# Performance work log

Measured on AMD Instinct MI355X. Metric: run time of the kernel, lower is better.

## Reference

```python
import jax, jax.numpy as jnp
import numpy as np

BN_EPS = 1e-5


def _knn_idx(pos, k):
    # pos: (B, 3, N). Nearest-k by squared euclidean distance (self included).
    sq = jnp.sum(pos * pos, axis=1)                        # (B, N)
    inner = jnp.einsum('bcn,bcm->bnm', pos, pos)           # (B, N, N)
    neg_dist = 2.0 * inner - sq[:, :, None] - sq[:, None, :]
    _, idx = jax.lax.top_k(neg_dist, k)                    # (B, N, k)
    return idx


def setup_inputs() -> dict:
    key = jax.random.key(0)
    k1, k2, k3 = jax.random.split(key, 3)
    B, C, N, K, D = 4, 64, 8192, 16, 64
    return {
        'x': jax.random.normal(k1, (B, C, N), dtype=jnp.float32),
        'pos': jax.random.normal(k2, (B, 3, N), dtype=jnp.float32),
        'spectral_filter': jax.random.normal(k3, (K, C, D), dtype=jnp.float32),
        'gamma': jnp.ones((D,), dtype=jnp.float32),
        'beta': jnp.zeros((D,), dtype=jnp.float32),
    }


def reference(x, pos, spectral_filter, gamma, beta):
    k = spectral_filter.shape[0]
    idx = _knn_idx(pos, k)                                  # (B, N, k) int32
    # gather neighbors: nb[b, c, n, j] = x[b, c, idx[b, n, j]]
    nb = jax.vmap(lambda xf, ii: xf[:, ii])(x, idx)         # (B, C, N, k)
    edge = nb - x[:, :, :, None]                            # (B, C, N, k)
    # per-k small GEMM: 'bnkc,kcd->bnd' (channel dim is axis 1 here)
    out = jnp.einsum('bcnk,kcd->bnd', edge, spectral_filter)
    out = out.transpose(0, 2, 1)                            # (B, D, N)
    # BatchNorm1d, training mode (biased variance over batch and points)
    mean = jnp.mean(out, axis=(0, 2), keepdims=True)
    var = jnp.var(out, axis=(0, 2), keepdims=True)
    out = (out - mean) * jax.lax.rsqrt(var + BN_EPS)
    return out * gamma[None, :, None] + beta[None, :, None]
```

## Files before the change

kernel.cpp:

```cpp
#include <hip/hip_runtime.h>
#include <hip/hip_bf16.h>

#define NPTS 8192
#define NQ   32768
#define KNN  16
#define SCAP 112

#define OFF_XT   0
#define OFF_FBIG (8*1024*1024)
#define OFF_SUMS (OFF_FBIG + 278528)
#define OFF_IDX  (OFF_SUMS + 512)
#define OFF_PRE  (OFF_IDX + 2*1024*1024)
#define OFF_SQ   OFF_PRE

__device__ __forceinline__ float sq3(float x, float y, float z) {
    #pragma clang fp contract(off)
    float xx = x * x;
    float yy = y * y;
    float zz = z * z;
    return (xx + yy) + zz;
}
__device__ __forceinline__ float negd2(float qx, float qy, float qz, float sqn,
                                       float mx, float my, float mz, float sqm) {
    #pragma clang fp contract(off)
    float p0 = qx * mx;
    float inn = __builtin_fmaf(qz, mz, __builtin_fmaf(qy, my, p0));
    float t = 2.0f * inn;
    float u = t - sqn;
    return u - sqm;
}
#define KEY_EPS2 2.0e-3f

__global__ __launch_bounds__(256) void k_prep(const float* __restrict__ x,
                                              const float* __restrict__ F,
                                              const float* __restrict__ pos,
                                              float* __restrict__ xT,
                                              float* __restrict__ Fb,
                                              float* __restrict__ sums,
                                              float* __restrict__ sqa) {
    int bid = blockIdx.x;
    if (bid < 512) {
        __shared__ float tile[64][65];
        int lane = threadIdx.x & 63, wid = threadIdx.x >> 6;
        int b = bid >> 7, nt = bid & 127;
        int n0 = nt * 64;
        for (int rr = 0; rr < 16; ++rr) {
            int c = wid * 16 + rr;
            tile[c][lane] = x[((size_t)b * 64 + c) * NPTS + n0 + lane];
        }
        __syncthreads();
        for (int rr = 0; rr < 16; ++rr) {
            int r = wid * 16 + rr;
            xT[((size_t)(b * NPTS + n0 + r)) * 64 + lane] = tile[lane][r];
        }
    } else if (bid < 528) {
        int j = bid - 512;
        for (int e = threadIdx.x; e < 4096; e += 256)
            Fb[j * 4096 + e] = F[j * 4096 + e];
    } else if (bid == 528) {
        for (int e = threadIdx.x; e < 4096; e += 256) {
            float s = 0.f;
            for (int k = 0; k < 16; ++k) s += F[k * 4096 + e];
            Fb[16 * 4096 + e] = -s;
        }
    } else if (bid == 529) {
        if (threadIdx.x < 128) sums[threadIdx.x] = 0.f;
    } else {
        int g = (bid - 530) * 256 + threadIdx.x;
        int b = g >> 13, n = g & (NPTS - 1);
        const float* pb = pos + (size_t)b * 3 * NPTS;
        sqa[g] = sq3(pb[n], pb[NPTS + n], pb[2 * NPTS + n]);
    }
}

__global__ __launch_bounds__(256, 4) void k_knn(const float* __restrict__ pos,
                                                const float* __restrict__ sqa,
                                                int* __restrict__ idxo) {
    __shared__ int            cnt[32];
    __shared__ unsigned short sidx[32][SCAP];
    __shared__ float          skey[32][SCAP];
    __shared__ int            outI[32][16];
    int t = threadIdx.x, lane = t & 63, wid = t >> 6;
    int qblk = blockIdx.x * 32;
    int b = qblk >> 13;
    const float* px = pos + (size_t)b * 3 * NPTS;
    const float* py = px + NPTS;
    const float* pz = py + NPTS;
    const float* sb = sqa + (size_t)b * NPTS;
    int n0 = (qblk & (NPTS - 1)) + wid * 8;

    float qxs[8], qys[8], qzs[8], sqs[8], tqx[8], tqy[8], tqz[8];
    #pragma unroll
    for (int i = 0; i < 8; ++i) {
        qxs[i] = px[n0 + i]; qys[i] = py[n0 + i]; qzs[i] = pz[n0 + i];
        sqs[i] = sb[n0 + i];
        tqx[i] = 2.0f * qxs[i]; tqy[i] = 2.0f * qys[i]; tqz[i] = 2.0f * qzs[i];
    }
    if (lane < 8) cnt[wid * 8 + lane] = 0;
    if (lane < 16) {
        #pragma unroll
        for (int i = 0; i < 8; ++i) outI[wid * 8 + i][lane] = n0 + i;
    }

    float lm[8];
    #pragma unroll
    for (int i = 0; i < 8; ++i) lm[i] = -3.4e38f;
    for (int it = 0; it < 32; ++it) {
        int m = it * 256 + lane * 4;
        float4 X = *(const float4*)(px + m);
        float4 Y = *(const float4*)(py + m);
        float4 Z = *(const float4*)(pz + m);
        float4 S = *(const float4*)(sb + m);
        #pragma unroll
        for (int i = 0; i < 8; ++i) {
            float a0 = __builtin_fmaf(tqx[i], X.x, __builtin_fmaf(tqy[i], Y.x, __builtin_fmaf(tqz[i], Z.x, -S.x)));
            float a1 = __builtin_fmaf(tqx[i], X.y, __builtin_fmaf(tqy[i], Y.y, __builtin_fmaf(tqz[i], Z.y, -S.y)));
            float a2 = __builtin_fmaf(tqx[i], X.z, __builtin_fmaf(tqy[i], Y.z, __builtin_fmaf(tqz[i], Z.z, -S.z)));
            float a3 = __builtin_fmaf(tqx[i], X.w, __builtin_fmaf(tqy[i], Y.w, __builtin_fmaf(tqz[i], Z.w, -S.w)));
            float m012 = fmaxf(fmaxf(a0, a1), a2);
            lm[i] = fmaxf(fmaxf(m012, a3), lm[i]);
        }
    }

    float thr[8];
    #pragma unroll
    for (int i = 0; i < 8; ++i) {
        float val = lm[i], tv = 0.f;
        for (int r = 0; r < 16; ++r) {
            float mm = val;
            mm = fmaxf(mm, __shfl_xor(mm, 1, 64));
            mm = fmaxf(mm, __shfl_xor(mm, 2, 64));
            mm = fmaxf(mm, __shfl_xor(mm, 4, 64));
            mm = fmaxf(mm, __shfl_xor(mm, 8, 64));
            mm = fmaxf(mm, __shfl_xor(mm, 16, 64));
            mm = fmaxf(mm, __shfl_xor(mm, 32, 64));
            tv = mm;
            if (val == mm) val = -3.4e38f;
        }
        thr[i] = tv - KEY_EPS2;
    }

    for (int it = 0; it < 32; ++it) {
        int m = it * 256 + lane * 4;
        float4 X = *(const float4*)(px + m);
        float4 Y = *(const float4*)(py + m);
        float4 Z = *(const float4*)(pz + m);
        float4 S = *(const float4*)(sb + m);
        #pragma unroll
        for (int i = 0; i < 8; ++i) {
            int lq = wid * 8 + i;
            float a0 = __builtin_fmaf(tqx[i], X.x, __builtin_fmaf(tqy[i], Y.x, __builtin_fmaf(tqz[i], Z.x, -S.x)));
            float a1 = __builtin_fmaf(tqx[i], X.y, __builtin_fmaf(tqy[i], Y.y, __builtin_fmaf(tqz[i], Z.y, -S.y)));
            float a2 = __builtin_fmaf(tqx[i], X.z, __builtin_fmaf(tqy[i], Y.z, __builtin_fmaf(tqz[i], Z.z, -S.z)));
            float a3 = __builtin_fmaf(tqx[i], X.w, __builtin_fmaf(tqy[i], Y.w, __builtin_fmaf(tqz[i], Z.w, -S.w)));
            if (a0 >= thr[i]) { int s_ = atomicAdd(&cnt[lq],1); if (s_<SCAP) sidx[lq][s_] = (unsigned short)m; }
            if (a1 >= thr[i]) { int s_ = atomicAdd(&cnt[lq],1); if (s_<SCAP) sidx[lq][s_] = (unsigned short)(m+1); }
            if (a2 >= thr[i]) { int s_ = atomicAdd(&cnt[lq],1); if (s_<SCAP) sidx[lq][s_] = (unsigned short)(m+2); }
            if (a3 >= thr[i]) { int s_ = atomicAdd(&cnt[lq],1); if (s_<SCAP) sidx[lq][s_] = (unsigned short)(m+3); }
        }
    }

    #pragma unroll 1
    for (int i = 0; i < 8; ++i) {
        int lq = wid * 8 + i;
        int S = cnt[lq]; if (S > SCAP) S = SCAP;
        for (int p = lane; p < S; p += 64) {
            int m = sidx[lq][p];
            skey[lq][p] = negd2(qxs[i], qys[i], qzs[i], sqs[i],
                                px[m], py[m], pz[m], sb[m]);
        }
    }

    #pragma unroll 1
    for (int i = 0; i < 8; ++i) {
        int lq = wid * 8 + i;
        int S = cnt[lq]; if (S > SCAP) S = SCAP;
        for (int p = lane; p < S; p += 64) {
            int m = sidx[lq][p];
            float km = skey[lq][p];
            int rank = 0;
            for (int j = 0; j < S; ++j) {
                float kj = skey[lq][j];
                int ij = sidx[lq][j];
                if (kj > km || (kj == km && ij < m)) rank++;
            }
            if (rank < KNN) outI[lq][rank] = m;
        }
    }
    __syncthreads();
    #pragma unroll
    for (int h = 0; h < 2; ++h) {
        int lq = h * 16 + (t >> 4);
        idxo[(size_t)(qblk + lq) * KNN + (t & 15)] = outI[lq][t & 15];
    }
}

#define CPAD 68
__global__ __launch_bounds__(256) void k_conv(const float* __restrict__ xT,
                                              const float* __restrict__ Fb,
                                              const int* __restrict__ idx,
                                              float* __restrict__ outp,
                                              float* __restrict__ sums) {
    __shared__ float At[64][CPAD];
    __shared__ float Bt[64 * 64];
    int t = threadIdx.x;
    int q0 = blockIdx.x * 64;
    int bbase = q0 & ~(NPTS - 1);
    int qi0 = (t >> 4) * 4;
    int dj0 = (t & 15) * 4;
    int r = t & 63;
    int s = t >> 6;

    float acc[4][4];
    #pragma unroll
    for (int a = 0; a < 4; ++a)
        #pragma unroll
        for (int bb = 0; bb < 4; ++bb) acc[a][bb] = 0.f;

    for (int j = 0; j < 17; ++j) {
        {
            int qg = q0 + r;
            int nbr = (j < 16) ? (idx[(size_t)qg * KNN + j] & (NPTS - 1))
                               : (qg & (NPTS - 1));
            const float* src = xT + ((size_t)(bbase + nbr) * 64 + s * 16);
            float4 v0 = *(const float4*)(src);
            float4 v1 = *(const float4*)(src + 4);
            float4 v2 = *(const float4*)(src + 8);
            float4 v3 = *(const float4*)(src + 12);
            int c0 = s * 16;
            At[c0+ 0][r] = v0.x; At[c0+ 1][r] = v0.y; At[c0+ 2][r] = v0.z; At[c0+ 3][r] = v0.w;
            At[c0+ 4][r] = v1.x; At[c0+ 5][r] = v1.y; At[c0+ 6][r] = v1.z; At[c0+ 7][r] = v1.w;
            At[c0+ 8][r] = v2.x; At[c0+ 9][r] = v2.y; At[c0+10][r] = v2.z; At[c0+11][r] = v2.w;
            At[c0+12][r] = v3.x; At[c0+13][r] = v3.y; At[c0+14][r] = v3.z; At[c0+15][r] = v3.w;
        }
        {
            const float* fj = Fb + j * 4096;
            #pragma unroll
            for (int u = 0; u < 4; ++u) {
                int e = u * 1024 + t * 4;
                *(float4*)&Bt[e] = *(const float4*)(fj + e);
            }
        }
        __syncthreads();
        #pragma unroll 8
        for (int k = 0; k < 64; ++k) {
            float4 av = *(const float4*)&At[k][qi0];
            float4 bv = *(const float4*)&Bt[k * 64 + dj0];
            acc[0][0] = fmaf(av.x, bv.x, acc[0][0]);
            acc[0][1] = fmaf(av.x, bv.y, acc[0][1]);
            acc[0][2] = fmaf(av.x, bv.z, acc[0][2]);
            acc[0][3] = fmaf(av.x, bv.w, acc[0][3]);
            acc[1][0] = fmaf(av.y, bv.x, acc[1][0]);
            acc[1][1] = fmaf(av.y, bv.y, acc[1][1]);
            acc[1][2] = fmaf(av.y, bv.z, acc[1][2]);
            acc[1][3] = fmaf(av.y, bv.w, acc[1][3]);
            acc[2][0] = fmaf(av.z, bv.x, acc[2][0]);
            acc[2][1] = fmaf(av.z, bv.y, acc[2][1]);
            acc[2][2] = fmaf(av.z, bv.z, acc[2][2]);
            acc[2][3] = fmaf(av.z, bv.w, acc[2][3]);
            acc[3][0] = fmaf(av.w, bv.x, acc[3][0]);
            acc[3][1] = fmaf(av.w, bv.y, acc[3][1]);
            acc[3][2] = fmaf(av.w, bv.z, acc[3][2]);
            acc[3][3] = fmaf(av.w, bv.w, acc[3][3]);
        }
        __syncthreads();
    }
    #pragma unroll
    for (int qi = 0; qi < 4; ++qi) {
        float4 o = make_float4(acc[qi][0], acc[qi][1], acc[qi][2], acc[qi][3]);
        *(float4*)(outp + (size_t)(q0 + qi0 + qi) * 64 + dj0) = o;
    }
    {
        float* P  = Bt;
        float* P2 = Bt + 1024;
        int g = t >> 4;
        #pragma unroll
        for (int dd = 0; dd < 4; ++dd) {
            float sv = ((acc[0][dd] + acc[1][dd]) + acc[2][dd]) + acc[3][dd];
            float qv = fmaf(acc[3][dd], acc[3][dd],
                       fmaf(acc[2][dd], acc[2][dd],
                       fmaf(acc[1][dd], acc[1][dd], acc[0][dd] * acc[0][dd])));
            P [g * 64 + dj0 + dd] = sv;
            P2[g * 64 + dj0 + dd] = qv;
        }
        __syncthreads();
        if (t < 64) {
            float a = 0.f, b2 = 0.f;
            #pragma unroll
            for (int gg = 0; gg < 16; ++gg) {
                a  += P [gg * 64 + t];
                b2 += P2[gg * 64 + t];
            }
            atomicAdd(&sums[t], a);
            atomicAdd(&sums[64 + t], b2);
        }
    }
}

__global__ __launch_bounds__(256) void k_bn(const float* __restrict__ outp,
                                            const float* __restrict__ sums,
                                            const float* __restrict__ gamma,
                                            const float* __restrict__ beta,
                                            float* __restrict__ out) {
    __shared__ float tile[64][65];
    __shared__ float sa[64], sb[64];
    int lane = threadIdx.x & 63, wid = threadIdx.x >> 6;
    int b = blockIdx.x >> 7, nt = blockIdx.x & 127;
    int n0 = nt * 64;
    if (threadIdx.x < 64) {
        const float inv = 1.f / 32768.f;
        float mean = sums[threadIdx.x] * inv;
        float var = sums[64 + threadIdx.x] * inv - mean * mean;
        float rs = rsqrtf(var + 1e-5f);
        float a = rs * gamma[threadIdx.x];
        sa[threadIdx.x] = a;
        sb[threadIdx.x] = beta[threadIdx.x] - mean * a;
    }
    for (int rr = 0; rr < 16; ++rr) {
        int r = wid * 16 + rr;
        tile[r][lane] = outp[((size_t)(b * NPTS + n0 + r)) * 64 + lane];
    }
    __syncthreads();
    for (int rr = 0; rr < 16; ++rr) {
        int dr = wid * 16 + rr;
        out[((size_t)b * 64 + dr) * NPTS + n0 + lane] =
            fmaf(tile[lane][dr], sa[dr], sb[dr]);
    }
}

extern "C" void kernel_launch(void* const* d_in, const int* in_sizes, int n_in,
                              void* d_out, int out_size, void* d_ws, size_t ws_size,
                              hipStream_t stream) {
    (void)in_sizes; (void)n_in; (void)out_size; (void)ws_size;
    const float* x     = (const float*)d_in[0];
    const float* pos   = (const float*)d_in[1];
    const float* F     = (const float*)d_in[2];
    const float* gamma = (const float*)d_in[3];
    const float* beta  = (const float*)d_in[4];
    float* out = (float*)d_out;

    char* ws = (char*)d_ws;
    float* xT   = (float*)(ws + OFF_XT);
    float* Fb   = (float*)(ws + OFF_FBIG);
    float* sums = (float*)(ws + OFF_SUMS);
    int*   idx  = (int*)(ws + OFF_IDX);
    float* pre  = (float*)(ws + OFF_PRE);
    float* sqa  = (float*)(ws + OFF_SQ);

    k_prep<<<658, 256, 0, stream>>>(x, F, pos, xT, Fb, sums, sqa);
    k_knn<<<1024, 256, 0, stream>>>(pos, sqa, idx);
    k_conv<<<512, 256, 0, stream>>>(xT, Fb, idx, pre, sums);
    k_bn<<<512, 256, 0, stream>>>(pre, sums, gamma, beta, out);
}
```

Before: 282.8 us.

## Pack KNN distance math into float2 ops and enlarge conv register tile

The KNN scan now computes distances for pairs of queries with two-wide vector FMA and max, which MI355X can issue as packed FP32 instructions, aiming to halve the VALU instruction count in both passes. The conv kernel drops to 128 threads per block, with each thread accumulating an 8x4 output tile instead of 4x4, so each shared-memory load feeds more FMAs. The trade-off is higher register pressure and fewer threads per block to hide the latency of the neighbor gathers. It also risks changing how the rounding of distance keys near the threshold behaves, although the FMA order is kept.

```diff
diff --git a/kernel.cpp b/kernel.cpp
--- a/kernel.cpp
+++ b/kernel.cpp
@@ -12,6 +12,15 @@
 #define OFF_IDX  (OFF_SUMS + 512)
 #define OFF_PRE  (OFF_IDX + 2*1024*1024)
 #define OFF_SQ   OFF_PRE
+
+typedef float v2f __attribute__((ext_vector_type(2)));
+__device__ __forceinline__ v2f sp2(float v) { return (v2f){v, v}; }
+__device__ __forceinline__ v2f fma2(v2f a, v2f b, v2f c) {
+    return __builtin_elementwise_fma(a, b, c);
+}
+__device__ __forceinline__ v2f max2(v2f a, v2f b) {
+    return __builtin_elementwise_max(a, b);
+}
 
 __device__ __forceinline__ float sq3(float x, float y, float z) {
     #pragma clang fp contract(off)
@@ -89,12 +98,18 @@
     const float* sb = sqa + (size_t)b * NPTS;
     int n0 = (qblk & (NPTS - 1)) + wid * 8;
 
-    float qxs[8], qys[8], qzs[8], sqs[8], tqx[8], tqy[8], tqz[8];
+    float qxs[8], qys[8], qzs[8], sqs[8];
     #pragma unroll
     for (int i = 0; i < 8; ++i) {
         qxs[i] = px[n0 + i]; qys[i] = py[n0 + i]; qzs[i] = pz[n0 + i];
         sqs[i] = sb[n0 + i];
-        tqx[i] = 2.0f * qxs[i]; tqy[i] = 2.0f * qys[i]; tqz[i] = 2.0f * qzs[i];
+    }
+    v2f tqx2[4], tqy2[4], tqz2[4];
+    #pragma unroll
+    for (int p = 0; p < 4; ++p) {
+        tqx2[p] = (v2f){2.0f * qxs[2*p], 2.0f * qxs[2*p+1]};
+        tqy2[p] = (v2f){2.0f * qys[2*p], 2.0f * qys[2*p+1]};
+        tqz2[p] = (v2f){2.0f * qzs[2*p], 2.0f * qzs[2*p+1]};
     }
     if (lane < 8) cnt[wid * 8 + lane] = 0;
     if (lane < 16) {
@@ -102,30 +117,32 @@
         for (int i = 0; i < 8; ++i) outI[wid * 8 + i][lane] = n0 + i;
     }
 
-    float lm[8];
-    #pragma unroll
-    for (int i = 0; i < 8; ++i) lm[i] = -3.4e38f;
+    v2f lm2[4];
+    #pragma unroll
+    for (int p = 0; p < 4; ++p) lm2[p] = sp2(-3.4e38f);
     for (int it = 0; it < 32; ++it) {
         int m = it * 256 + lane * 4;
         float4 X = *(const float4*)(px + m);
         float4 Y = *(const float4*)(py + m);
         float4 Z = *(const float4*)(pz + m);
         float4 S = *(const float4*)(sb + m);
-        #pragma unroll
-        for (int i = 0; i < 8; ++i) {
-            float a0 = __builtin_fmaf(tqx[i], X.x, __builtin_fmaf(tqy[i], Y.x, __builtin_fmaf(tqz[i], Z.x, -S.x)));
-            float a1 = __builtin_fmaf(tqx[i], X.y, __builtin_fmaf(tqy[i], Y.y, __builtin_fmaf(tqz[i], Z.y, -S.y)));
-            float a2 = __builtin_fmaf(tqx[i], X.z, __builtin_fmaf(tqy[i], Y.z, __builtin_fmaf(tqz[i], Z.z, -S.z)));
-            float a3 = __builtin_fmaf(tqx[i], X.w, __builtin_fmaf(tqy[i], Y.w, __builtin_fmaf(tqz[i], Z.w, -S.w)));
-            float m012 = fmaxf(fmaxf(a0, a1), a2);
-            lm[i] = fmaxf(fmaxf(m012, a3), lm[i]);
+        float n0s = -S.x, n1s = -S.y, n2s = -S.z, n3s = -S.w;
+        #pragma unroll
+        for (int p = 0; p < 4; ++p) {
+            v2f k0 = fma2(tqx2[p], sp2(X.x), fma2(tqy2[p], sp2(Y.x), fma2(tqz2[p], sp2(Z.x), sp2(n0s))));
+            v2f k1 = fma2(tqx2[p], sp2(X.y), fma2(tqy2[p], sp2(Y.y), fma2(tqz2[p], sp2(Z.y), sp2(n1s))));
+            v2f k2 = fma2(tqx2[p], sp2(X.z), fma2(tqy2[p], sp2(Y.z), fma2(tqz2[p], sp2(Z.z), sp2(n2s))));
+            v2f k3 = fma2(tqx2[p], sp2(X.w), fma2(tqy2[p], sp2(Y.w), fma2(tqz2[p], sp2(Z.w), sp2(n3s))));
+            v2f m01 = max2(k0, k1), m23 = max2(k2, k3);
+            lm2[p] = max2(lm2[p], max2(m01, m23));
         }
     }
 
     float thr[8];
     #pragma unroll
     for (int i = 0; i < 8; ++i) {
-        float val = lm[i], tv = 0.f;
+        float val = (i & 1) ? lm2[i >> 1].y : lm2[i >> 1].x;
+        float tv = 0.f;
         for (int r = 0; r < 16; ++r) {
             float mm = val;
             mm = fmaxf(mm, __shfl_xor(mm, 1, 64));
@@ -146,17 +163,23 @@
         float4 Y = *(const float4*)(py + m);
         float4 Z = *(const float4*)(pz + m);
         float4 S = *(const float4*)(sb + m);
-        #pragma unroll
-        for (int i = 0; i < 8; ++i) {
-            int lq = wid * 8 + i;
-            float a0 = __builtin_fmaf(tqx[i], X.x, __builtin_fmaf(tqy[i], Y.x, __builtin_fmaf(tqz[i], Z.x, -S.x)));
-            float a1 = __builtin_fmaf(tqx[i], X.y, __builtin_fmaf(tqy[i], Y.y, __builtin_fmaf(tqz[i], Z.y, -S.y)));
-            float a2 = __builtin_fmaf(tqx[i], X.z, __builtin_fmaf(tqy[i], Y.z, __builtin_fmaf(tqz[i], Z.z, -S.z)));
-            float a3 = __builtin_fmaf(tqx[i], X.w, __builtin_fmaf(tqy[i], Y.w, __builtin_fmaf(tqz[i], Z.w, -S.w)));
-            if (a0 >= thr[i]) { int s_ = atomicAdd(&cnt[lq],1); if (s_<SCAP) sidx[lq][s_] = (unsigned short)m; }
-            if (a1 >= thr[i]) { int s_ = atomicAdd(&cnt[lq],1); if (s_<SCAP) sidx[lq][s_] = (unsigned short)(m+1); }
-            if (a2 >= thr[i]) { int s_ = atomicAdd(&cnt[lq],1); if (s_<SCAP) sidx[lq][s_] = (unsigned short)(m+2); }
-            if (a3 >= thr[i]) { int s_ = atomicAdd(&cnt[lq],1); if (s_<SCAP) sidx[lq][s_] = (unsigned short)(m+3); }
+        float n0s = -S.x, n1s = -S.y, n2s = -S.z, n3s = -S.w;
+        #pragma unroll
+        for (int p = 0; p < 4; ++p) {
+            int lq0 = wid * 8 + 2 * p, lq1 = lq0 + 1;
+            float t0 = thr[2*p], t1 = thr[2*p+1];
+            v2f k0 = fma2(tqx2[p], sp2(X.x), fma2(tqy2[p], sp2(Y.x), fma2(tqz2[p], sp2(Z.x), sp2(n0s))));
+            v2f k1 = fma2(tqx2[p], sp2(X.y), fma2(tqy2[p], sp2(Y.y), fma2(tqz2[p], sp2(Z.y), sp2(n1s))));
+            v2f k2 = fma2(tqx2[p], sp2(X.z), fma2(tqy2[p], sp2(Y.z), fma2(tqz2[p], sp2(Z.z), sp2(n2s))));
+            v2f k3 = fma2(tqx2[p], sp2(X.w), fma2(tqy2[p], sp2(Y.w), fma2(tqz2[p], sp2(Z.w), sp2(n3s))));
+            if (k0.x >= t0) { int s_ = atomicAdd(&cnt[lq0],1); if (s_<SCAP) sidx[lq0][s_] = (unsigned short)m; }
+            if (k1.x >= t0) { int s_ = atomicAdd(&cnt[lq0],1); if (s_<SCAP) sidx[lq0][s_] = (unsigned short)(m+1); }
+            if (k2.x >= t0) { int s_ = atomicAdd(&cnt[lq0],1); if (s_<SCAP) sidx[lq0][s_] = (unsigned short)(m+2); }
+            if (k3.x >= t0) { int s_ = atomicAdd(&cnt[lq0],1); if (s_<SCAP) sidx[lq0][s_] = (unsigned short)(m+3); }
+            if (k0.y >= t1) { int s_ = atomicAdd(&cnt[lq1],1); if (s_<SCAP) sidx[lq1][s_] = (unsigned short)m; }
+            if (k1.y >= t1) { int s_ = atomicAdd(&cnt[lq1],1); if (s_<SCAP) sidx[lq1][s_] = (unsigned short)(m+1); }
+            if (k2.y >= t1) { int s_ = atomicAdd(&cnt[lq1],1); if (s_<SCAP) sidx[lq1][s_] = (unsigned short)(m+2); }
+            if (k3.y >= t1) { int s_ = atomicAdd(&cnt[lq1],1); if (s_<SCAP) sidx[lq1][s_] = (unsigned short)(m+3); }
         }
     }
 
@@ -196,7 +219,7 @@
 }
 
 #define CPAD 68
-__global__ __launch_bounds__(256) void k_conv(const float* __restrict__ xT,
+__global__ __launch_bounds__(128) void k_conv(const float* __restrict__ xT,
                                               const float* __restrict__ Fb,
                                               const int* __restrict__ idx,
                                               float* __restrict__ outp,
@@ -206,14 +229,14 @@
     int t = threadIdx.x;
     int q0 = blockIdx.x * 64;
     int bbase = q0 & ~(NPTS - 1);
-    int qi0 = (t >> 4) * 4;
+    int qi0 = (t >> 4) * 8;
     int dj0 = (t & 15) * 4;
     int r = t & 63;
-    int s = t >> 6;
-
-    float acc[4][4];
-    #pragma unroll
-    for (int a = 0; a < 4; ++a)
+    int h = t >> 6;
+
+    float acc[8][4];
+    #pragma unroll
+    for (int a = 0; a < 8; ++a)
         #pragma unroll
         for (int bb = 0; bb < 4; ++bb) acc[a][bb] = 0.f;
 
@@ -222,64 +245,60 @@
             int qg = q0 + r;
             int nbr = (j < 16) ? (idx[(size_t)qg * KNN + j] & (NPTS - 1))
                                : (qg & (NPTS - 1));
-            const float* src = xT + ((size_t)(bbase + nbr) * 64 + s * 16);
-            float4 v0 = *(const float4*)(src);
-            float4 v1 = *(const float4*)(src + 4);
-            float4 v2 = *(const float4*)(src + 8);
-            float4 v3 = *(const float4*)(src + 12);
-            int c0 = s * 16;
-            At[c0+ 0][r] = v0.x; At[c0+ 1][r] = v0.y; At[c0+ 2][r] = v0.z; At[c0+ 3][r] = v0.w;
-            At[c0+ 4][r] = v1.x; At[c0+ 5][r] = v1.y; At[c0+ 6][r] = v1.z; At[c0+ 7][r] = v1.w;
-            At[c0+ 8][r] = v2.x; At[c0+ 9][r] = v2.y; At[c0+10][r] = v2.z; At[c0+11][r] = v2.w;
-            At[c0+12][r] = v3.x; At[c0+13][r] = v3.y; At[c0+14][r] = v3.z; At[c0+15][r] = v3.w;
+            const float* src = xT + ((size_t)(bbase + nbr) * 64 + h * 32);
+            #pragma unroll
+            for (int s = 0; s < 8; ++s) {
+                float4 v = *(const float4*)(src + s * 4);
+                int c0 = h * 32 + s * 4;
+                At[c0 + 0][r] = v.x;
+                At[c0 + 1][r] = v.y;
+                At[c0 + 2][r] = v.z;
+                At[c0 + 3][r] = v.w;
+            }
         }
         {
             const float* fj = Fb + j * 4096;
             #pragma unroll
-            for (int u = 0; u < 4; ++u) {
-                int e = u * 1024 + t * 4;
+            for (int u = 0; u < 8; ++u) {
+                int e = u * 512 + t * 4;
                 *(float4*)&Bt[e] = *(const float4*)(fj + e);
             }
         }
         __syncthreads();
         #pragma unroll 8
         for (int k = 0; k < 64; ++k) {
-            float4 av = *(const float4*)&At[k][qi0];
+            float4 a0 = *(const float4*)&At[k][qi0];
+            float4 a1 = *(const float4*)&At[k][qi0 + 4];
             float4 bv = *(const float4*)&Bt[k * 64 + dj0];
-            acc[0][0] = fmaf(av.x, bv.x, acc[0][0]);
-            acc[0][1] = fmaf(av.x, bv.y, acc[0][1]);
-            acc[0][2] = fmaf(av.x, bv.z, acc[0][2]);
-            acc[0][3] = fmaf(av.x, bv.w, acc[0][3]);
-            acc[1][0] = fmaf(av.y, bv.x, acc[1][0]);
-            acc[1][1] = fmaf(av.y, bv.y, acc[1][1]);
-            acc[1][2] = fmaf(av.y, bv.z, acc[1][2]);
-            acc[1][3] = fmaf(av.y, bv.w, acc[1][3]);
-            acc[2][0] = fmaf(av.z, bv.x, acc[2][0]);
-            acc[2][1] = fmaf(av.z, bv.y, acc[2][1]);
-            acc[2][2] = fmaf(av.z, bv.z, acc[2][2]);
-            acc[2][3] = fmaf(av.z, bv.w, acc[2][3]);
-            acc[3][0] = fmaf(av.w, bv.x, acc[3][0]);
-            acc[3][1] = fmaf(av.w, bv.y, acc[3][1]);
-            acc[3][2] = fmaf(av.w, bv.z, acc[3][2]);
-            acc[3][3] = fmaf(av.w, bv.w, acc[3][3]);
+            float aq[8] = {a0.x, a0.y, a0.z, a0.w, a1.x, a1.y, a1.z, a1.w};
+            #pragma unroll
+            for (int qq = 0; qq < 8; ++qq) {
+                acc[qq][0] = fmaf(aq[qq], bv.x, acc[qq][0]);
+                acc[qq][1] = fmaf(aq[qq], bv.y, acc[qq][1]);
+                acc[qq][2] = fmaf(aq[qq], bv.z, acc[qq][2]);
+                acc[qq][3] = fmaf(aq[qq], bv.w, acc[qq][3]);
+            }
         }
         __syncthreads();
     }
     #pragma unroll
-    for (int qi = 0; qi < 4; ++qi) {
-        float4 o = make_float4(acc[qi][0], acc[qi][1], acc[qi][2], acc[qi][3]);
-        *(float4*)(outp + (size_t)(q0 + qi0 + qi) * 64 + dj0) = o;
+    for (int qq = 0; qq < 8; ++qq) {
+        float4 o = make_float4(acc[qq][0], acc[qq][1], acc[qq][2], acc[qq][3]);
+        *(float4*)(outp + (size_t)(q0 + qi0 + qq) * 64 + dj0) = o;
     }
     {
         float* P  = Bt;
-        float* P2 = Bt + 1024;
+        float* P2 = Bt + 512;
         int g = t >> 4;
         #pragma unroll
         for (int dd = 0; dd < 4; ++dd) {
-            float sv = ((acc[0][dd] + acc[1][dd]) + acc[2][dd]) + acc[3][dd];
-            float qv = fmaf(acc[3][dd], acc[3][dd],
-                       fmaf(acc[2][dd], acc[2][dd],
-                       fmaf(acc[1][dd], acc[1][dd], acc[0][dd] * acc[0][dd])));
+            float sv = acc[0][dd];
+            float qv = acc[0][dd] * acc[0][dd];
+            #pragma unroll
+            for (int qq = 1; qq < 8; ++qq) {
+                sv += acc[qq][dd];
+                qv = fmaf(acc[qq][dd], acc[qq][dd], qv);
+            }
             P [g * 64 + dj0 + dd] = sv;
             P2[g * 64 + dj0 + dd] = qv;
         }
@@ -287,7 +306,7 @@
         if (t < 64) {
             float a = 0.f, b2 = 0.f;
             #pragma unroll
-            for (int gg = 0; gg < 16; ++gg) {
+            for (int gg = 0; gg < 8; ++gg) {
                 a  += P [gg * 64 + t];
                 b2 += P2[gg * 64 + t];
             }
@@ -349,6 +368,6 @@
 
     k_prep<<<658, 256, 0, stream>>>(x, F, pos, xT, Fb, sums, sqa);
     k_knn<<<1024, 256, 0, stream>>>(pos, sqa, idx);
-    k_conv<<<512, 256, 0, stream>>>(xT, Fb, idx, pre, sums);
+    k_conv<<<512, 128, 0, stream>>>(xT, Fb, idx, pre, sums);
     k_bn<<<512, 256, 0, stream>>>(pre, sums, gamma, beta, out);
 }
```

New measurement: 315.3 us. +11.5%, slower.

## Split kNN candidate scan across two waves per query group

Applied to the files above, without the earlier changes.

Each kNN block now handles 16 queries instead of 32, and two waves share each group of 8 queries, each scanning half of the points. Each half computes a local 16th-best threshold; the two are exchanged through shared memory and the larger is used as the filter. The grid doubles, launch bounds rise to 8 blocks per CU, and the key and rank phases are redistributed at 4 queries per wave. This shortens the per-wave serial scan and raises occupancy. The cost is extra block-wide barriers, and a threshold taken from one half may let more candidates through, which could overflow the fixed candidate buffer.

```diff
diff --git a/kernel.cpp b/kernel.cpp
--- a/kernel.cpp
+++ b/kernel.cpp
@@ -73,40 +73,40 @@
     }
 }
 
-__global__ __launch_bounds__(256, 4) void k_knn(const float* __restrict__ pos,
+__global__ __launch_bounds__(256, 8) void k_knn(const float* __restrict__ pos,
                                                 const float* __restrict__ sqa,
                                                 int* __restrict__ idxo) {
-    __shared__ int            cnt[32];
-    __shared__ unsigned short sidx[32][SCAP];
-    __shared__ float          skey[32][SCAP];
-    __shared__ int            outI[32][16];
+    __shared__ int            cnt[16];
+    __shared__ unsigned short sidx[16][SCAP];
+    __shared__ float          skey[16][SCAP];
+    __shared__ int            outI[16][16];
+    __shared__ float          taus[16][2];
     int t = threadIdx.x, lane = t & 63, wid = t >> 6;
-    int qblk = blockIdx.x * 32;
+    int grp = wid >> 1, half = wid & 1;
+    int qblk = blockIdx.x * 16;
     int b = qblk >> 13;
     const float* px = pos + (size_t)b * 3 * NPTS;
     const float* py = px + NPTS;
     const float* pz = py + NPTS;
     const float* sb = sqa + (size_t)b * NPTS;
-    int n0 = (qblk & (NPTS - 1)) + wid * 8;
-
-    float qxs[8], qys[8], qzs[8], sqs[8], tqx[8], tqy[8], tqz[8];
+    int nbase = qblk & (NPTS - 1);
+    int n0 = nbase + grp * 8;
+
+    float tqx[8], tqy[8], tqz[8];
     #pragma unroll
     for (int i = 0; i < 8; ++i) {
-        qxs[i] = px[n0 + i]; qys[i] = py[n0 + i]; qzs[i] = pz[n0 + i];
-        sqs[i] = sb[n0 + i];
-        tqx[i] = 2.0f * qxs[i]; tqy[i] = 2.0f * qys[i]; tqz[i] = 2.0f * qzs[i];
-    }
-    if (lane < 8) cnt[wid * 8 + lane] = 0;
-    if (lane < 16) {
-        #pragma unroll
-        for (int i = 0; i < 8; ++i) outI[wid * 8 + i][lane] = n0 + i;
-    }
+        tqx[i] = 2.0f * px[n0 + i];
+        tqy[i] = 2.0f * py[n0 + i];
+        tqz[i] = 2.0f * pz[n0 + i];
+    }
+    if (t < 16) cnt[t] = 0;
+    outI[t >> 4][t & 15] = nbase + (t >> 4);
 
     float lm[8];
     #pragma unroll
     for (int i = 0; i < 8; ++i) lm[i] = -3.4e38f;
-    for (int it = 0; it < 32; ++it) {
-        int m = it * 256 + lane * 4;
+    for (int it = 0; it < 16; ++it) {
+        int m = half * 4096 + it * 256 + lane * 4;
         float4 X = *(const float4*)(px + m);
         float4 Y = *(const float4*)(py + m);
         float4 Z = *(const float4*)(pz + m);
@@ -122,7 +122,6 @@
         }
     }
 
-    float thr[8];
     #pragma unroll
     for (int i = 0; i < 8; ++i) {
         float val = lm[i], tv = 0.f;
@@ -137,18 +136,24 @@
             tv = mm;
             if (val == mm) val = -3.4e38f;
         }
-        thr[i] = tv - KEY_EPS2;
-    }
-
-    for (int it = 0; it < 32; ++it) {
-        int m = it * 256 + lane * 4;
+        if (lane == 0) taus[grp * 8 + i][half] = tv;
+    }
+    __syncthreads();
+
+    float thr[8];
+    #pragma unroll
+    for (int i = 0; i < 8; ++i)
+        thr[i] = fmaxf(taus[grp * 8 + i][0], taus[grp * 8 + i][1]) - KEY_EPS2;
+
+    for (int it = 0; it < 16; ++it) {
+        int m = half * 4096 + it * 256 + lane * 4;
         float4 X = *(const float4*)(px + m);
         float4 Y = *(const float4*)(py + m);
         float4 Z = *(const float4*)(pz + m);
         float4 S = *(const float4*)(sb + m);
         #pragma unroll
         for (int i = 0; i < 8; ++i) {
-            int lq = wid * 8 + i;
+            int lq = grp * 8 + i;
             float a0 = __builtin_fmaf(tqx[i], X.x, __builtin_fmaf(tqy[i], Y.x, __builtin_fmaf(tqz[i], Z.x, -S.x)));
             float a1 = __builtin_fmaf(tqx[i], X.y, __builtin_fmaf(tqy[i], Y.y, __builtin_fmaf(tqz[i], Z.y, -S.y)));
             float a2 = __builtin_fmaf(tqx[i], X.z, __builtin_fmaf(tqy[i], Y.z, __builtin_fmaf(tqz[i], Z.z, -S.z)));
@@ -159,21 +164,24 @@
             if (a3 >= thr[i]) { int s_ = atomicAdd(&cnt[lq],1); if (s_<SCAP) sidx[lq][s_] = (unsigned short)(m+3); }
         }
     }
+    __syncthreads();
 
     #pragma unroll 1
-    for (int i = 0; i < 8; ++i) {
-        int lq = wid * 8 + i;
+    for (int i = 0; i < 4; ++i) {
+        int lq = wid * 4 + i;
+        int qn = nbase + lq;
+        float qx = px[qn], qy = py[qn], qz = pz[qn], sqn = sb[qn];
         int S = cnt[lq]; if (S > SCAP) S = SCAP;
         for (int p = lane; p < S; p += 64) {
             int m = sidx[lq][p];
-            skey[lq][p] = negd2(qxs[i], qys[i], qzs[i], sqs[i],
-                                px[m], py[m], pz[m], sb[m]);
-        }
-    }
+            skey[lq][p] = negd2(qx, qy, qz, sqn, px[m], py[m], pz[m], sb[m]);
+        }
+    }
+    __syncthreads();
 
     #pragma unroll 1
-    for (int i = 0; i < 8; ++i) {
-        int lq = wid * 8 + i;
+    for (int i = 0; i < 4; ++i) {
+        int lq = wid * 4 + i;
         int S = cnt[lq]; if (S > SCAP) S = SCAP;
         for (int p = lane; p < S; p += 64) {
             int m = sidx[lq][p];
@@ -188,11 +196,7 @@
         }
     }
     __syncthreads();
-    #pragma unroll
-    for (int h = 0; h < 2; ++h) {
-        int lq = h * 16 + (t >> 4);
-        idxo[(size_t)(qblk + lq) * KNN + (t & 15)] = outI[lq][t & 15];
-    }
+    idxo[(size_t)(qblk + (t >> 4)) * KNN + (t & 15)] = outI[t >> 4][t & 15];
 }
 
 #define CPAD 68
@@ -348,7 +352,7 @@
     float* sqa  = (float*)(ws + OFF_SQ);
 
     k_prep<<<658, 256, 0, stream>>>(x, F, pos, xT, Fb, sums, sqa);
-    k_knn<<<1024, 256, 0, stream>>>(pos, sqa, idx);
+    k_knn<<<2048, 256, 0, stream>>>(pos, sqa, idx);
     k_conv<<<512, 256, 0, stream>>>(xT, Fb, idx, pre, sums);
     k_bn<<<512, 256, 0, stream>>>(pre, sums, gamma, beta, out);
 }
```

Result: slower. 296.6 us (+4.9%).
